# Kernel optimization log

Measured on AMD Instinct MI355X. Metric: run time of the kernel, lower is better.

Reference implementation:

```python
import jax, jax.numpy as jnp
import numpy as np

B=4; L=1024; NF=64; DM=256; DS=16; SCS=8; NL=4; DI=512; DTR=16; DC=4; NFM=6; NH=4; SCALES=(5,20,50)

def _ln(x,g,b):
    m=x.mean(-1,keepdims=True); v=((x-m)**2).mean(-1,keepdims=True)
    return (x-m)*jax.lax.rsqrt(v+1e-5)*g+b

def _scan(dA,dBu,C):
    # sequential selective scan: h_t = dA_t*h + dBu_t ; y_t = sum_n h_t * C_t
    def step(h,inp):
        a,bu,c=inp
        h=a*h+bu
        return h, jnp.einsum('bdn,bn->bd',h,c)
    h0=jnp.zeros(dA.shape[:1]+dA.shape[2:],dA.dtype)
    _,ys=jax.lax.scan(step,h0,(dA.swapaxes(0,1),dBu.swapaxes(0,1),C.swapaxes(0,1)))
    return ys.swapaxes(0,1)  # [B,L,DI]

def _mamba(x,g,b,inw,cw,cb,xpw,dtw,dtb,Alog,Dp,outw,ds):
    # MambaBlock: LN -> SelectiveSSM -> residual (dropout=identity in eval)
    xn=_ln(x,g,b)
    u,z=jnp.split(xn@inw.T,2,-1)
    k=cw.T[:,None,:]  # torch depthwise Conv1d weight [DI,1,DC] -> WIO [DC,1,DI]
    u=jax.lax.conv_general_dilated(u,k,(1,),[(cw.shape[1]-1,0)],dimension_numbers=('NWC','WIO','NWC'),feature_group_count=u.shape[-1])+cb
    u=jax.nn.silu(u)
    A=-jnp.exp(Alog)                     # [DI,ds]
    xd=u@xpw.T                           # [B,L,DTR+2*ds]
    dt=jax.nn.softplus(xd[...,:DTR]@dtw.T+dtb)   # [B,L,DI]
    Bm=xd[...,DTR:DTR+ds]; Cm=xd[...,DTR+ds:]
    dA=jnp.exp(dt[...,None]*A)                   # [B,L,DI,ds]
    dBu=dt[...,None]*Bm[:,:,None,:]*u[...,None]  # [B,L,DI,ds]
    y=_scan(dA,dBu,Cm)+u*Dp
    return x+(y*jax.nn.silu(z))@outw.T

def _mha(x,wqkv,bqkv,wout,bout):
    Bq,S,E=x.shape; hd=E//NH
    q,k,v=jnp.split(x@wqkv.T+bqkv,3,-1)
    sp=lambda t: t.reshape(Bq,S,NH,hd).transpose(0,2,1,3)
    att=jax.nn.softmax(jnp.einsum('bhqd,bhkd->bhqk',sp(q),sp(k))*(1.0/np.sqrt(hd)),-1)
    o=jnp.einsum('bhqk,bhkd->bhqd',att,sp(v)).transpose(0,2,1,3).reshape(Bq,S,E)
    return o@wout.T+bout

def _forward(x,in_w,in_b,in_ln_g,in_ln_b,mb_ln_g,mb_ln_b,mb_in_w,mb_conv_w,mb_conv_b,mb_xp_w,mb_dt_w,mb_dt_b,mb_Alog,mb_D,mb_out_w,sc_ln_g,sc_ln_b,sc_in_w,sc_conv_w,sc_conv_b,sc_xp_w,sc_dt_w,sc_dt_b,sc_Alog,sc_D,sc_out_w,fus_qkv_w,fus_qkv_b,fus_out_w,fus_out_b,ms_out_w,ms_out_b,sa_ln1_g,sa_ln1_b,sa_ln2_g,sa_ln2_b,sa_qkv_w,sa_qkv_b,sa_out_w,sa_out_b,sa_ff1_w,sa_ff1_b,sa_ff2_w,sa_ff2_b,ev1_w,ev1_b,ev2_w,ev2_b,ttf1_w,ttf1_b,ttf2_w,ttf2_b,emb_w,emb_b):
    gelu=lambda t: jax.nn.gelu(t,approximate=False)
    h=gelu(_ln(x@in_w.T+in_b,in_ln_g,in_ln_b))
    for i in range(NL):
        h=_mamba(h,mb_ln_g[i],mb_ln_b[i],mb_in_w[i],mb_conv_w[i],mb_conv_b[i],mb_xp_w[i],mb_dt_w[i],mb_dt_b[i],mb_Alog[i],mb_D[i],mb_out_w[i],DS)
    pooled=[]
    for i,s in enumerate(SCALES):
        p=_mamba(h[:,-s:,:],sc_ln_g[i],sc_ln_b[i],sc_in_w[i],sc_conv_w[i],sc_conv_b[i],sc_xp_w[i],sc_dt_w[i],sc_dt_b[i],sc_Alog[i],sc_D[i],sc_out_w[i],SCS)
        pooled.append(p.mean(1))  # AdaptiveAvgPool1d(1)
    stack=jnp.stack(pooled,1)  # [B,3,DM]
    fused=_mha(stack,fus_qkv_w,fus_qkv_b,fus_out_w,fus_out_b).reshape(x.shape[0],-1)@ms_out_w.T+ms_out_b
    s2=stack+_mha(_ln(stack,sa_ln1_g,sa_ln1_b),sa_qkv_w,sa_qkv_b,sa_out_w,sa_out_b)
    att=s2+(gelu(_ln(s2,sa_ln2_g,sa_ln2_b)@sa_ff1_w.T+sa_ff1_b)@sa_ff2_w.T+sa_ff2_b)
    final=fused+att.mean(1)
    ev=jax.nn.softplus(gelu(final@ev1_w.T+ev1_b)@ev2_w.T+ev2_b)
    alpha=ev+1.0
    Ssum=alpha.sum(-1,keepdims=True)
    probs=alpha/Ssum; unc=(NFM+1)/Ssum
    ttf=gelu(final@ttf1_w.T+ttf1_b)@ttf2_w.T+ttf2_b
    tm=jax.nn.softplus(ttf[:,:NFM]); ts=jnp.exp(0.5*ttf[:,NFM:])
    emb=final@emb_w.T+emb_b
    # concat of (probs, evidence, alpha, uncertainty, ttf_mean, ttf_std, embedding) -> [B,162]
    return jnp.concatenate([probs,ev,alpha,unc,tm,ts,emb],-1)

def setup_inputs():
    ks=iter(jax.random.split(jax.random.key(0),64))
    nk=lambda: next(ks)
    w=lambda *s: jax.random.normal(nk(),s,jnp.float32)*0.02
    z=lambda *s: jnp.zeros(s,jnp.float32)
    o=lambda *s: jnp.ones(s,jnp.float32)
    Al=lambda n,ds: jnp.broadcast_to(jnp.log(jnp.arange(1,ds+1,dtype=jnp.float32)),(n,DI,ds))
    return dict(x=jax.random.normal(nk(),(B,L,NF),jnp.float32),
        in_w=w(DM,NF), in_b=z(DM), in_ln_g=o(DM), in_ln_b=z(DM),
        mb_ln_g=o(NL,DM), mb_ln_b=z(NL,DM), mb_in_w=w(NL,2*DI,DM), mb_conv_w=w(NL,DI,DC), mb_conv_b=z(NL,DI),
        mb_xp_w=w(NL,DTR+2*DS,DI), mb_dt_w=w(NL,DI,DTR), mb_dt_b=z(NL,DI), mb_Alog=Al(NL,DS), mb_D=o(NL,DI), mb_out_w=w(NL,DM,DI),
        sc_ln_g=o(3,DM), sc_ln_b=z(3,DM), sc_in_w=w(3,2*DI,DM), sc_conv_w=w(3,DI,DC), sc_conv_b=z(3,DI),
        sc_xp_w=w(3,DTR+2*SCS,DI), sc_dt_w=w(3,DI,DTR), sc_dt_b=z(3,DI), sc_Alog=Al(3,SCS), sc_D=o(3,DI), sc_out_w=w(3,DM,DI),
        fus_qkv_w=w(3*DM,DM), fus_qkv_b=z(3*DM), fus_out_w=w(DM,DM), fus_out_b=z(DM), ms_out_w=w(DM,3*DM), ms_out_b=z(DM),
        sa_ln1_g=o(DM), sa_ln1_b=z(DM), sa_ln2_g=o(DM), sa_ln2_b=z(DM),
        sa_qkv_w=w(3*DM,DM), sa_qkv_b=z(3*DM), sa_out_w=w(DM,DM), sa_out_b=z(DM),
        sa_ff1_w=w(4*DM,DM), sa_ff1_b=z(4*DM), sa_ff2_w=w(DM,4*DM), sa_ff2_b=z(DM),
        ev1_w=w(DM,DM), ev1_b=z(DM), ev2_w=w(NFM+1,DM), ev2_b=z(NFM+1),
        ttf1_w=w(DM//2,DM), ttf1_b=z(DM//2), ttf2_w=w(2*NFM,DM//2), ttf2_b=z(2*NFM),
        emb_w=w(DM//2,DM), emb_b=z(DM//2))

def reference(x,in_w,in_b,in_ln_g,in_ln_b,mb_ln_g,mb_ln_b,mb_in_w,mb_conv_w,mb_conv_b,mb_xp_w,mb_dt_w,mb_dt_b,mb_Alog,mb_D,mb_out_w,sc_ln_g,sc_ln_b,sc_in_w,sc_conv_w,sc_conv_b,sc_xp_w,sc_dt_w,sc_dt_b,sc_Alog,sc_D,sc_out_w,fus_qkv_w,fus_qkv_b,fus_out_w,fus_out_b,ms_out_w,ms_out_b,sa_ln1_g,sa_ln1_b,sa_ln2_g,sa_ln2_b,sa_qkv_w,sa_qkv_b,sa_out_w,sa_out_b,sa_ff1_w,sa_ff1_b,sa_ff2_w,sa_ff2_b,ev1_w,ev1_b,ev2_w,ev2_b,ttf1_w,ttf1_b,ttf2_w,ttf2_b,emb_w,emb_b):
    return _forward(x,in_w,in_b,in_ln_g,in_ln_b,mb_ln_g,mb_ln_b,mb_in_w,mb_conv_w,mb_conv_b,mb_xp_w,mb_dt_w,mb_dt_b,mb_Alog,mb_D,mb_out_w,sc_ln_g,sc_ln_b,sc_in_w,sc_conv_w,sc_conv_b,sc_xp_w,sc_dt_w,sc_dt_b,sc_Alog,sc_D,sc_out_w,fus_qkv_w,fus_qkv_b,fus_out_w,fus_out_b,ms_out_w,ms_out_b,sa_ln1_g,sa_ln1_b,sa_ln2_g,sa_ln2_b,sa_qkv_w,sa_qkv_b,sa_out_w,sa_out_b,sa_ff1_w,sa_ff1_b,sa_ff2_w,sa_ff2_b,ev1_w,ev1_b,ev2_w,ev2_b,ttf1_w,ttf1_b,ttf2_w,ttf2_b,emb_w,emb_b)
```

## Files before the change

kernel.cpp:

```cpp
#include <hip/hip_runtime.h>
#include <math.h>


typedef short short8v __attribute__((ext_vector_type(8)));
typedef float f32x4   __attribute__((ext_vector_type(4)));

__device__ __forceinline__ float geluf(float x){ return 0.5f*x*(1.0f + erff(x*0.70710678118654752f)); }
__device__ __forceinline__ float softplusf_(float x){ return (x > 20.f) ? x : log1pf(expf(x)); }
__device__ __forceinline__ unsigned short f2bf(float f){
  unsigned int u = __float_as_uint(f);
  unsigned int r = (u + 0x7FFFu + ((u >> 16) & 1u)) >> 16;
  return (unsigned short)r;
}

__global__ __launch_bounds__(256) void k_f2b_all(
    const float* s0, unsigned short* d0,
    const float* s1, unsigned short* d1,
    const float* s2, unsigned short* d2,
    const float* s3, unsigned short* d3,
    const float* s4, unsigned short* d4,
    const float* s5, unsigned short* d5)
{
  int blk = blockIdx.x;
  const float* s; unsigned short* d; int base;
  if      (blk < 1024){ s=s0; d=d0; base=0; }
  else if (blk < 1536){ s=s1; d=d1; base=1024; }
  else if (blk < 1632){ s=s2; d=d2; base=1536; }
  else if (blk < 2400){ s=s3; d=d3; base=1632; }
  else if (blk < 2784){ s=s4; d=d4; base=2400; }
  else                { s=s5; d=d5; base=2784; }
  int i = ((blk - base)*256 + threadIdx.x)*4;
  float4 v = *(const float4*)(s + i);
  *(ushort4*)(d + i) = make_ushort4(f2bf(v.x), f2bf(v.y), f2bf(v.z), f2bf(v.w));
}

__global__ __launch_bounds__(256) void k_inproj(
    const float* __restrict__ x, const float* __restrict__ w,
    const float* __restrict__ b, const float* __restrict__ g,
    const float* __restrict__ beta, float* __restrict__ h)
{
  __shared__ float xr[64];
  __shared__ float r1[4], r2[4];
  int row = blockIdx.x;
  int tid = threadIdx.x;
  if (tid < 64) xr[tid] = x[row*64 + tid];
  __syncthreads();
  float acc = b[tid];
  const float* wr = w + tid*64;
  #pragma unroll
  for (int k = 0; k < 64; k++) acc += xr[k]*wr[k];
  float s1 = acc, s2 = acc*acc;
  #pragma unroll
  for (int o = 32; o > 0; o >>= 1){ s1 += __shfl_down(s1,o,64); s2 += __shfl_down(s2,o,64); }
  if ((tid & 63) == 0){ r1[tid>>6] = s1; r2[tid>>6] = s2; }
  __syncthreads();
  float S1 = r1[0]+r1[1]+r1[2]+r1[3];
  float S2 = r2[0]+r2[1]+r2[2]+r2[3];
  float m = S1*(1.f/256.f);
  float var = S2*(1.f/256.f) - m*m;
  float xn = (acc - m)*rsqrtf(var + 1e-5f)*g[tid] + beta[tid];
  h[row*256 + tid] = geluf(xn);
}

__global__ __launch_bounds__(256) void k_ln(
    const float* __restrict__ src, const float* __restrict__ g, const float* __restrict__ beta,
    unsigned short* __restrict__ dst)
{
  __shared__ float r1[4], r2[4];
  int r = blockIdx.x, tid = threadIdx.x;
  float v = src[r*256 + tid];
  float s1 = v, s2 = v*v;
  #pragma unroll
  for (int o = 32; o > 0; o >>= 1){ s1 += __shfl_down(s1,o,64); s2 += __shfl_down(s2,o,64); }
  if ((tid & 63) == 0){ r1[tid>>6] = s1; r2[tid>>6] = s2; }
  __syncthreads();
  float S1 = r1[0]+r1[1]+r1[2]+r1[3];
  float S2 = r2[0]+r2[1]+r2[2]+r2[3];
  float m = S1*(1.f/256.f);
  float var = S2*(1.f/256.f) - m*m;
  dst[r*256 + tid] = f2bf((v - m)*rsqrtf(var + 1e-5f)*g[tid] + beta[tid]);
}

__device__ __forceinline__ void sc_region(int r, int& z, int& roff, int& s){
  if (r < 64){ z=0; roff=0; s=5; }
  else if (r < 192){ z=1; roff=64; s=20; }
  else { z=2; roff=192; s=50; }
}

__global__ __launch_bounds__(256) void k_ln_sc(
    const float* __restrict__ h, const float* __restrict__ gb, const float* __restrict__ bb,
    unsigned short* __restrict__ dst)
{
  __shared__ float r1[4], r2[4];
  int r = blockIdx.x, tid = threadIdx.x;
  int z, roff, s; sc_region(r, z, roff, s);
  int local = r - roff;
  if (local >= 4*s) return;
  int b = local / s, t = local % s;
  float v = h[(b*1024 + (1024 - s) + t)*256 + tid];
  const float* g = gb + z*256; const float* be = bb + z*256;
  float s1 = v, s2 = v*v;
  #pragma unroll
  for (int o = 32; o > 0; o >>= 1){ s1 += __shfl_down(s1,o,64); s2 += __shfl_down(s2,o,64); }
  if ((tid & 63) == 0){ r1[tid>>6] = s1; r2[tid>>6] = s2; }
  __syncthreads();
  float S1 = r1[0]+r1[1]+r1[2]+r1[3];
  float S2 = r2[0]+r2[1]+r2[2]+r2[3];
  float m = S1*(1.f/256.f);
  float var = S2*(1.f/256.f) - m*m;
  dst[r*256 + tid] = f2bf((v - m)*rsqrtf(var + 1e-5f)*g[tid] + be[tid]);
}

template<int MODE, int SCB>
__global__ __launch_bounds__(256) void k_mm64(
    const unsigned short* __restrict__ A, const unsigned short* __restrict__ Wb,
    float* __restrict__ C,
    const float* __restrict__ resid,
    float* __restrict__ pool_out,
    int M, int N, int K, int wstr)
{
  int tid = threadIdx.x;
  int wave = tid >> 6, lane = tid & 63;
  int mh = wave & 1, nh = wave >> 1;
  int m0 = blockIdx.y*64 + mh*32;
  int n0 = blockIdx.x*64 + nh*32;
  int z = 0, roff = 0, sc = 0;
  const unsigned short* W = Wb;
  if (SCB){ sc_region(blockIdx.y*64, z, roff, sc); W += z*wstr; }
  int lrow = lane & 15, kc = lane >> 4;
  f32x4 acc[2][2] = {{{0.f,0.f,0.f,0.f},{0.f,0.f,0.f,0.f}},{{0.f,0.f,0.f,0.f},{0.f,0.f,0.f,0.f}}};
  for (int k0 = 0; k0 < K; k0 += 32){
    short8v a[2], b[2];
    #pragma unroll
    for (int mi = 0; mi < 2; mi++){
      int r = m0 + mi*16 + lrow; r = min(r, M-1);
      a[mi] = *(const short8v*)(A + r*K + k0 + kc*8);
    }
    #pragma unroll
    for (int ni = 0; ni < 2; ni++){
      int c = n0 + ni*16 + lrow;
      b[ni] = *(const short8v*)(W + c*K + k0 + kc*8);
    }
    #pragma unroll
    for (int mi = 0; mi < 2; mi++)
      #pragma unroll
      for (int ni = 0; ni < 2; ni++)
        acc[mi][ni] = __builtin_amdgcn_mfma_f32_16x16x32_bf16(a[mi], b[ni], acc[mi][ni], 0, 0, 0);
  }
  int rb = kc*4;
  #pragma unroll
  for (int mi = 0; mi < 2; mi++){
    #pragma unroll
    for (int rr = 0; rr < 4; rr++){
      int grow = m0 + mi*16 + rb + rr;
      if (grow >= M) continue;
      #pragma unroll
      for (int ni = 0; ni < 2; ni++){
        int gcol = n0 + ni*16 + lrow;
        float v = acc[mi][ni][rr];
        if (MODE == 0){
          C[grow*N + gcol] = v;
        } else if (MODE == 1){
          C[grow*N + gcol] = resid[grow*256 + gcol] + v;
        } else {
          int local = grow - roff;
          if (local < 4*sc){
            int bb2 = local / sc, t = local % sc;
            float rv = resid[(bb2*1024 + (1024 - sc) + t)*256 + gcol] + v;
            atomicAdd(&pool_out[bb2*768 + z*256 + gcol], rv*(1.f/(float)sc));
          }
        }
      }
    }
  }
}

template<int NT, int SCB>
__global__ __launch_bounds__(256) void k_xpdt(
    const unsigned short* __restrict__ A, const unsigned short* __restrict__ Wb,
    float* __restrict__ xdout,
    const float* __restrict__ dtwb, const float* __restrict__ dtbb,
    float* __restrict__ dtout, int M)
{
  const int K = 512;
  const int NC = NT*16;
  __shared__ float pacc[4][16][NC];
  __shared__ float sxd[16][16];
  int tid = threadIdx.x;
  int wave = tid >> 6, lane = tid & 63;
  int bm0 = blockIdx.x*16;
  const unsigned short* W = Wb;
  const float* dtw = dtwb;
  const float* dtb = dtbb;
  if (SCB){
    int z, roff, s; sc_region(bm0, z, roff, s);
    W += z*(NC*K); dtw += z*8192; dtb += z*512;
  }
  int lrow = lane & 15, kc = lane >> 4;
  int kbase = wave*128;
  f32x4 acc[NT];
  #pragma unroll
  for (int ni = 0; ni < NT; ni++) acc[ni] = (f32x4){0.f,0.f,0.f,0.f};
  #pragma unroll
  for (int k0 = 0; k0 < 128; k0 += 32){
    short8v a = *(const short8v*)(A + (bm0 + lrow)*K + kbase + k0 + kc*8);
    #pragma unroll
    for (int ni = 0; ni < NT; ni++){
      short8v b = *(const short8v*)(W + (ni*16 + lrow)*K + kbase + k0 + kc*8);
      acc[ni] = __builtin_amdgcn_mfma_f32_16x16x32_bf16(a, b, acc[ni], 0, 0, 0);
    }
  }
  int rb = kc*4;
  #pragma unroll
  for (int rr = 0; rr < 4; rr++)
    #pragma unroll
    for (int ni = 0; ni < NT; ni++)
      pacc[wave][rb + rr][ni*16 + lrow] = acc[ni][rr];
  __syncthreads();
  for (int e = tid; e < 16*NC; e += 256){
    int r = e / NC, c = e % NC;
    float v = pacc[0][r][c] + pacc[1][r][c] + pacc[2][r][c] + pacc[3][r][c];
    xdout[(bm0 + r)*NC + c] = v;
    if (c < 16) sxd[r][c] = v;
  }
  __syncthreads();
  int d0 = tid, d1 = tid + 256;
  float w0[16], w1[16];
  #pragma unroll
  for (int j = 0; j < 16; j++){ w0[j] = dtw[d0*16 + j]; w1[j] = dtw[d1*16 + j]; }
  float b0 = dtb[d0], b1 = dtb[d1];
  #pragma unroll
  for (int r = 0; r < 16; r++){
    float a0 = b0, a1 = b1;
    #pragma unroll
    for (int j = 0; j < 16; j++){
      float xv = sxd[r][j];
      a0 = fmaf(xv, w0[j], a0);
      a1 = fmaf(xv, w1[j], a1);
    }
    dtout[(bm0 + r)*512 + d0] = softplusf_(a0);
    dtout[(bm0 + r)*512 + d1] = softplusf_(a1);
  }
}

__global__ __launch_bounds__(256) void k_conv(
    const float* __restrict__ uz, const float* __restrict__ cw, const float* __restrict__ cb,
    float* __restrict__ uc, unsigned short* __restrict__ ucb)
{
  int row = blockIdx.x;
  int t = row & 1023;
  int tid = threadIdx.x;
  for (int d = tid; d < 512; d += 256){
    float acc = cb[d];
    const float* w = cw + d*4;
    #pragma unroll
    for (int k = 0; k < 4; k++){
      int ts = t - 3 + k;
      if (ts >= 0) acc += uz[(row - (3-k))*1024 + d]*w[k];
    }
    float s = acc/(1.f + expf(-acc));
    uc[row*512 + d] = s;
    ucb[row*512 + d] = f2bf(s);
  }
}

__global__ __launch_bounds__(256) void k_conv_sc(
    const float* __restrict__ uz, const float* __restrict__ cwb, const float* __restrict__ cbb,
    float* __restrict__ uc, unsigned short* __restrict__ ucb)
{
  int row = blockIdx.x;
  int z, roff, s; sc_region(row, z, roff, s);
  int local = row - roff;
  if (local >= 4*s) return;
  int t = local % s;
  const float* cw = cwb + z*2048;
  const float* cb = cbb + z*512;
  int tid = threadIdx.x;
  for (int d = tid; d < 512; d += 256){
    float acc = cb[d];
    const float* w = cw + d*4;
    #pragma unroll
    for (int k = 0; k < 4; k++){
      int ts = t - 3 + k;
      if (ts >= 0) acc += uz[(row - (3-k))*1024 + d]*w[k];
    }
    float sv = acc/(1.f + expf(-acc));
    uc[row*512 + d] = sv;
    ucb[row*512 + d] = f2bf(sv);
  }
}

__global__ __launch_bounds__(64) void k_scan_p1y(
    const float* __restrict__ dt, const float* __restrict__ uc,
    const float* __restrict__ xd, const float* __restrict__ Alog,
    float* __restrict__ hend, float* __restrict__ sdtb,
    float* __restrict__ yloc, float* __restrict__ Scum)
{
  const int CL = 64, NCH = 16;
  __shared__ float sdt[64][64], suc[64][64];
  __shared__ float sBC[64][32];
  int tid = threadIdx.x;
  int dblk = blockIdx.x;
  int d = dblk*64 + tid;
  int b = blockIdx.y, ch = blockIdx.z;
  int t0 = ch*CL;
  float A[16];
  #pragma unroll
  for (int n = 0; n < 16; n++) A[n] = -__expf(Alog[d*16 + n]);
  for (int e = tid; e < CL*16; e += 64){
    int t = e >> 4, q = (e & 15)*4;
    long off = (long)(b*1024 + t0 + t)*512 + dblk*64 + q;
    *(float4*)&sdt[t][q] = *(const float4*)(dt + off);
    *(float4*)&suc[t][q] = *(const float4*)(uc + off);
  }
  for (int e = tid; e < CL*8; e += 64){
    int t = e >> 3, q = (e & 7)*4;
    *(float4*)&sBC[t][q] = *(const float4*)(xd + (long)(b*1024 + t0 + t)*48 + 16 + q);
  }
  __syncthreads();
  float h[16];
  #pragma unroll
  for (int n = 0; n < 16; n++) h[n] = 0.f;
  float Ss = 0.f;
  #pragma unroll 2
  for (int t = 0; t < CL; t++){
    float dtv = sdt[t][tid];
    float uv  = suc[t][tid];
    Ss += dtv;
    float du = dtv*uv;
    float y = 0.f;
    #pragma unroll
    for (int n = 0; n < 16; n++){
      h[n] = fmaf(__expf(dtv*A[n]), h[n], du*sBC[t][n]);
      y = fmaf(h[n], sBC[t][16+n], y);
    }
    long row = (long)(b*1024 + t0 + t);
    yloc[row*512 + d] = y;
    Scum[row*512 + d] = Ss;
  }
  int base = ((b*NCH + ch)*512 + d)*16;
  #pragma unroll
  for (int q = 0; q < 4; q++)
    *(float4*)(hend + base + q*4) = make_float4(h[q*4], h[q*4+1], h[q*4+2], h[q*4+3]);
  sdtb[(b*NCH + ch)*512 + d] = Ss;
}

__global__ __launch_bounds__(256) void k_scomb(
    const float* __restrict__ hend, const float* __restrict__ sdtb,
    const float* __restrict__ Alog, float* __restrict__ hstart,
    float* __restrict__ Aneg)
{
  const int NCH = 16;
  int idx = blockIdx.x*256 + threadIdx.x;
  int low = idx & 8191;
  int d = (idx >> 4) & 511, b = idx >> 13;
  float A = -__expf(Alog[low]);
  if (b == 0) Aneg[low] = A;
  float hs = 0.f;
  hstart[(b*NCH)*8192 + low] = 0.f;
  for (int c = 0; c < NCH-1; c++){
    float S  = sdtb[(b*NCH + c)*512 + d];
    float he = hend[(b*NCH + c)*8192 + low];
    hs = fmaf(__expf(A*S), hs, he);
    hstart[(b*NCH + c + 1)*8192 + low] = hs;
  }
}

__global__ __launch_bounds__(256) void k_corr(
    const float* __restrict__ yloc, const float* __restrict__ Scum,
    const float* __restrict__ hstart, const float* __restrict__ Aneg,
    const float* __restrict__ xd, const float* __restrict__ uc,
    const float* __restrict__ uz, const float* __restrict__ Dp,
    unsigned short* __restrict__ yg)
{
  __shared__ float sC[16];
  int row = blockIdx.x, tid = threadIdx.x;
  int b = row >> 10, t = row & 1023, ch = t >> 6;
  if (tid < 16) sC[tid] = xd[row*48 + 32 + tid];
  __syncthreads();
  #pragma unroll
  for (int rep = 0; rep < 2; rep++){
    int d = tid + rep*256;
    float Ss = Scum[row*512 + d];
    float y  = yloc[row*512 + d];
    const float* hs = hstart + ((b*16 + ch)*512 + d)*16;
    const float* An = Aneg + d*16;
    #pragma unroll
    for (int n = 0; n < 16; n++)
      y = fmaf(__expf(An[n]*Ss)*hs[n], sC[n], y);
    float uv = uc[row*512 + d];
    y = fmaf(uv, Dp[d], y);
    float zv = uz[row*1024 + 512 + d];
    yg[row*512 + d] = f2bf(y*(zv/(1.f + __expf(-zv))));
  }
}

__global__ __launch_bounds__(64) void k_scan_sc(
    const float* __restrict__ dt, const float* __restrict__ uc,
    const float* __restrict__ uz, const float* __restrict__ xd,
    const float* __restrict__ Alogb, const float* __restrict__ Dpb,
    unsigned short* __restrict__ yg)
{
  __shared__ float sdt[52][64], suc[52][64], sz[52][64];
  __shared__ float sBC[52][16];
  int tid = threadIdx.x;
  int dblk = blockIdx.x;
  int d = dblk*64 + tid;
  int b = blockIdx.y, z = blockIdx.z;
  int s = (z==0) ? 5 : (z==1) ? 20 : 50;
  int roff = (z==0) ? 0 : (z==1) ? 64 : 192;
  const float* Alog = Alogb + z*4096;
  const float* Dp   = Dpb + z*512;
  float A[8];
  #pragma unroll
  for (int n = 0; n < 8; n++) A[n] = -__expf(Alog[d*8 + n]);
  float Dv = Dp[d];
  for (int e = tid; e < s*16; e += 64){
    int t = e >> 4, q = (e & 15)*4;
    long row = (long)(roff + b*s + t);
    *(float4*)&sdt[t][q] = *(const float4*)(dt + row*512 + dblk*64 + q);
    *(float4*)&suc[t][q] = *(const float4*)(uc + row*512 + dblk*64 + q);
    *(float4*)&sz[t][q]  = *(const float4*)(uz + row*1024 + 512 + dblk*64 + q);
  }
  for (int e = tid; e < s*4; e += 64){
    int t = e >> 2, q = (e & 3)*4;
    long row = (long)(roff + b*s + t);
    *(float4*)&sBC[t][q] = *(const float4*)(xd + row*32 + 16 + q);
  }
  __syncthreads();
  float h[8];
  #pragma unroll
  for (int n = 0; n < 8; n++) h[n] = 0.f;
  for (int t = 0; t < s; t++){
    float dtv = sdt[t][tid];
    float uv  = suc[t][tid];
    float zv  = sz[t][tid];
    float du = dtv*uv;
    float y = 0.f;
    #pragma unroll
    for (int n = 0; n < 8; n++){
      h[n] = fmaf(__expf(dtv*A[n]), h[n], du*sBC[t][n]);
      y = fmaf(h[n], sBC[t][8+n], y);
    }
    y = fmaf(uv, Dv, y);
    float gate = zv/(1.f + __expf(-zv));
    yg[(long)(roff + b*s + t)*512 + d] = f2bf(y*gate);
  }
}

__global__ void k_zero(float* p, int n){
  int i = blockIdx.x*256 + threadIdx.x;
  if (i < n) p[i] = 0.f;
}

template<int M, int ACT, int RES>
__global__ __launch_bounds__(256) void k_tw(
    const float* __restrict__ A, const float* __restrict__ W,
    const float* __restrict__ bias, float* __restrict__ out,
    const float* __restrict__ resid, int N, int K, int ostride, int ocoff)
{
  extern __shared__ float sx[];
  int tid = threadIdx.x;
  for (int e = tid*4; e < M*K; e += 1024)
    *(float4*)&sx[e] = *(const float4*)(A + e);
  __syncthreads();
  int wave = tid >> 6, lane = tid & 63;
  int c = blockIdx.x*4 + wave;
  if (c >= N) return;
  float acc[M];
  #pragma unroll
  for (int r = 0; r < M; r++) acc[r] = 0.f;
  for (int k = lane*4; k < K; k += 256){
    float4 w4 = *(const float4*)(W + c*K + k);
    #pragma unroll
    for (int r = 0; r < M; r++){
      float4 x4 = *(float4*)&sx[r*K + k];
      acc[r] = fmaf(x4.x,w4.x,fmaf(x4.y,w4.y,fmaf(x4.z,w4.z,fmaf(x4.w,w4.w,acc[r]))));
    }
  }
  #pragma unroll
  for (int r = 0; r < M; r++){
    #pragma unroll
    for (int o = 32; o > 0; o >>= 1) acc[r] += __shfl_down(acc[r], o, 64);
  }
  if (lane == 0){
    float bv = bias[c];
    #pragma unroll
    for (int r = 0; r < M; r++){
      float v = acc[r] + bv;
      if (ACT == 1) v = geluf(v);
      if (RES == 1) v += resid[r*256 + c];
      out[r*ostride + ocoff + c] = v;
    }
  }
}

__global__ __launch_bounds__(256) void k_t_ln(
    const float* __restrict__ src, const float* __restrict__ g, const float* __restrict__ b,
    float* __restrict__ dst)
{
  __shared__ float r1[4], r2[4];
  int r = blockIdx.x, tid = threadIdx.x;
  float v = src[r*256 + tid];
  float s1 = v, s2 = v*v;
  #pragma unroll
  for (int o = 32; o > 0; o >>= 1){ s1 += __shfl_down(s1,o,64); s2 += __shfl_down(s2,o,64); }
  if ((tid & 63) == 0){ r1[tid>>6] = s1; r2[tid>>6] = s2; }
  __syncthreads();
  float S1 = r1[0]+r1[1]+r1[2]+r1[3];
  float S2 = r2[0]+r2[1]+r2[2]+r2[3];
  float m = S1*(1.f/256.f);
  float var = S2*(1.f/256.f) - m*m;
  dst[r*256 + tid] = (v - m)*rsqrtf(var + 1e-5f)*g[tid] + b[tid];
}

__global__ __launch_bounds__(256) void k_t_att(
    const float* __restrict__ qkv, float* __restrict__ ov)
{
  __shared__ float att[36];
  int b = blockIdx.x, tid = threadIdx.x;
  if (tid < 36){
    int hh = tid/9, r = (tid%9)/3, c = tid%3;
    float s = 0.f;
    const float* qp = qkv + (b*3 + r)*768 + hh*64;
    const float* kp = qkv + (b*3 + c)*768 + 256 + hh*64;
    for (int k = 0; k < 64; k++) s += qp[k]*kp[k];
    att[hh*9 + r*3 + c] = s*0.125f;
  }
  __syncthreads();
  if (tid < 12){
    int hh = tid/3, r = tid%3;
    float a0 = att[hh*9+r*3+0], a1 = att[hh*9+r*3+1], a2 = att[hh*9+r*3+2];
    float m = fmaxf(a0, fmaxf(a1, a2));
    float e0 = expf(a0-m), e1 = expf(a1-m), e2 = expf(a2-m);
    float s = e0+e1+e2;
    att[hh*9+r*3+0] = e0/s; att[hh*9+r*3+1] = e1/s; att[hh*9+r*3+2] = e2/s;
  }
  __syncthreads();
  for (int e = tid; e < 768; e += 256){
    int p = e >> 8, i = e & 255, hh = i >> 6;
    ov[(b*3 + p)*256 + i] = att[hh*9+p*3+0]*qkv[(b*3+0)*768+512+i]
                          + att[hh*9+p*3+1]*qkv[(b*3+1)*768+512+i]
                          + att[hh*9+p*3+2]*qkv[(b*3+2)*768+512+i];
  }
}

__global__ __launch_bounds__(256) void k_t_final(
    const float* __restrict__ fusedv, const float* __restrict__ s2f, float* __restrict__ finalv)
{
  int b = blockIdx.x, c = threadIdx.x;
  finalv[b*256 + c] = fusedv[b*256 + c] +
    (s2f[(b*3+0)*256 + c] + s2f[(b*3+1)*256 + c] + s2f[(b*3+2)*256 + c])*(1.f/3.f);
}

__global__ __launch_bounds__(64) void k_t_fin(
    const float* __restrict__ evraw, const float* __restrict__ ttraw, float* __restrict__ out)
{
  __shared__ float ev[7];
  __shared__ float S;
  int b = blockIdx.x, tid = threadIdx.x;
  if (tid < 7) ev[tid] = softplusf_(evraw[b*7 + tid]);
  __syncthreads();
  if (tid == 0){
    float s = 0.f;
    for (int j = 0; j < 7; j++) s += ev[j] + 1.f;
    S = s;
  }
  __syncthreads();
  float* ob = out + b*162;
  if (tid < 7){
    float al = ev[tid] + 1.f;
    ob[tid] = al / S;
    ob[7 + tid] = ev[tid];
    ob[14 + tid] = al;
  }
  if (tid == 0) ob[21] = 7.f / S;
  if (tid < 6){
    ob[22 + tid] = softplusf_(ttraw[b*12 + tid]);
    ob[28 + tid] = expf(0.5f*ttraw[b*12 + 6 + tid]);
  }
}

extern "C" void kernel_launch(void* const* d_in, const int* in_sizes, int n_in,
                              void* d_out, int out_size, void* d_ws, size_t ws_size,
                              hipStream_t stream)
{
  const float* x         = (const float*)d_in[0];
  const float* in_w      = (const float*)d_in[1];
  const float* in_b      = (const float*)d_in[2];
  const float* in_ln_g   = (const float*)d_in[3];
  const float* in_ln_b   = (const float*)d_in[4];
  const float* mb_ln_g   = (const float*)d_in[5];
  const float* mb_ln_b   = (const float*)d_in[6];
  const float* mb_in_w   = (const float*)d_in[7];
  const float* mb_conv_w = (const float*)d_in[8];
  const float* mb_conv_b = (const float*)d_in[9];
  const float* mb_xp_w   = (const float*)d_in[10];
  const float* mb_dt_w   = (const float*)d_in[11];
  const float* mb_dt_b   = (const float*)d_in[12];
  const float* mb_Alog   = (const float*)d_in[13];
  const float* mb_D      = (const float*)d_in[14];
  const float* mb_out_w  = (const float*)d_in[15];
  const float* sc_ln_g   = (const float*)d_in[16];
  const float* sc_ln_b   = (const float*)d_in[17];
  const float* sc_in_w   = (const float*)d_in[18];
  const float* sc_conv_w = (const float*)d_in[19];
  const float* sc_conv_b = (const float*)d_in[20];
  const float* sc_xp_w   = (const float*)d_in[21];
  const float* sc_dt_w   = (const float*)d_in[22];
  const float* sc_dt_b   = (const float*)d_in[23];
  const float* sc_Alog   = (const float*)d_in[24];
  const float* sc_D      = (const float*)d_in[25];
  const float* sc_out_w  = (const float*)d_in[26];
  const float* fus_qkv_w = (const float*)d_in[27];
  const float* fus_qkv_b = (const float*)d_in[28];
  const float* fus_out_w = (const float*)d_in[29];
  const float* fus_out_b = (const float*)d_in[30];
  const float* ms_out_w  = (const float*)d_in[31];
  const float* ms_out_b  = (const float*)d_in[32];
  const float* sa_ln1_g  = (const float*)d_in[33];
  const float* sa_ln1_b  = (const float*)d_in[34];
  const float* sa_ln2_g  = (const float*)d_in[35];
  const float* sa_ln2_b  = (const float*)d_in[36];
  const float* sa_qkv_w  = (const float*)d_in[37];
  const float* sa_qkv_b  = (const float*)d_in[38];
  const float* sa_out_w  = (const float*)d_in[39];
  const float* sa_out_b  = (const float*)d_in[40];
  const float* sa_ff1_w  = (const float*)d_in[41];
  const float* sa_ff1_b  = (const float*)d_in[42];
  const float* sa_ff2_w  = (const float*)d_in[43];
  const float* sa_ff2_b  = (const float*)d_in[44];
  const float* ev1_w     = (const float*)d_in[45];
  const float* ev1_b     = (const float*)d_in[46];
  const float* ev2_w     = (const float*)d_in[47];
  const float* ev2_b     = (const float*)d_in[48];
  const float* ttf1_w    = (const float*)d_in[49];
  const float* ttf1_b    = (const float*)d_in[50];
  const float* ttf2_w    = (const float*)d_in[51];
  const float* ttf2_b    = (const float*)d_in[52];
  const float* emb_w     = (const float*)d_in[53];
  const float* emb_b     = (const float*)d_in[54];

  float* ws = (float*)d_ws;
  float* h     = ws;
  float* uz    = h    + 1048576;
  float* uc    = uz   + 4194304;
  float* dtb_  = uc   + 2097152;
  float* xd    = dtb_ + 2097152;
  float* stack = xd   + 196608;
  float* hend   = stack + 4096;
  float* hstart = hend + 524288;
  float* sdtb   = hstart + 524288;
  float* yloc   = sdtb + 32768;
  float* Scum   = yloc + 2097152;
  float* Aneg   = Scum + 2097152;
  float* qkvF   = Aneg + 8192;
  float* ovF    = qkvF + 9216;
  float* moF    = ovF  + 3072;
  float* fusedv = moF  + 3072;
  float* lnbuf  = fusedv + 1024;
  float* qkvS   = lnbuf + 3072;
  float* ovS    = qkvS + 9216;
  float* s2     = ovS  + 3072;
  float* ln2r   = s2   + 3072;
  float* hid    = ln2r + 3072;
  float* s2f    = hid  + 12288;
  float* finalv = s2f  + 3072;
  float* evh    = finalv + 1024;
  float* tth    = evh  + 1024;
  float* evraw  = tth  + 512;
  float* ttraw  = evraw + 32;
  float* fp32_end = ttraw + 64;
  unsigned short* bfb = (unsigned short*)fp32_end;
  unsigned short* xnb    = bfb;
  unsigned short* ucb    = xnb + 1048576;
  unsigned short* ygb    = ucb + 2097152;
  unsigned short* wmbin  = ygb + 2097152;
  unsigned short* wmbout = wmbin + 1048576;
  unsigned short* wmbxp  = wmbout + 524288;
  unsigned short* wscin  = wmbxp + 98304;
  unsigned short* wscout = wscin + 786432;
  unsigned short* wscxp  = wscout + 393216;

  k_f2b_all<<<2832, 256, 0, stream>>>(mb_in_w, wmbin, mb_out_w, wmbout, mb_xp_w, wmbxp,
                                      sc_in_w, wscin, sc_out_w, wscout, sc_xp_w, wscxp);

  k_inproj<<<4096, 256, 0, stream>>>(x, in_w, in_b, in_ln_g, in_ln_b, h);

  for (int l = 0; l < 4; l++){
    const float* Al = mb_Alog + l*8192;
    k_ln<<<4096, 256, 0, stream>>>(h, mb_ln_g + l*256, mb_ln_b + l*256, xnb);
    {
      dim3 g(16, 64);
      k_mm64<0,0><<<g, 256, 0, stream>>>(xnb, wmbin + l*262144, uz,
                                         nullptr, nullptr, 4096, 1024, 256, 0);
    }
    k_conv<<<4096, 256, 0, stream>>>(uz, mb_conv_w + l*2048, mb_conv_b + l*512, uc, ucb);
    k_xpdt<3,0><<<256, 256, 0, stream>>>(ucb, wmbxp + l*24576, xd,
                                         mb_dt_w + l*8192, mb_dt_b + l*512, dtb_, 4096);
    {
      dim3 g(8, 4, 16);
      k_scan_p1y<<<g, 64, 0, stream>>>(dtb_, uc, xd, Al, hend, sdtb, yloc, Scum);
      k_scomb<<<128, 256, 0, stream>>>(hend, sdtb, Al, hstart, Aneg);
      k_corr<<<4096, 256, 0, stream>>>(yloc, Scum, hstart, Aneg, xd, uc, uz,
                                       mb_D + l*512, ygb);
    }
    {
      dim3 g(4, 64);
      k_mm64<1,0><<<g, 256, 0, stream>>>(ygb, wmbout + l*131072, h,
                                         h, nullptr, 4096, 256, 512, 0);
    }
  }

  k_zero<<<12, 256, 0, stream>>>(stack, 3072);
  k_ln_sc<<<448, 256, 0, stream>>>(h, sc_ln_g, sc_ln_b, xnb);
  {
    dim3 g(16, 7);
    k_mm64<0,1><<<g, 256, 0, stream>>>(xnb, wscin, uz, nullptr, nullptr,
                                       448, 1024, 256, 262144);
  }
  k_conv_sc<<<448, 256, 0, stream>>>(uz, sc_conv_w, sc_conv_b, uc, ucb);
  k_xpdt<2,1><<<28, 256, 0, stream>>>(ucb, wscxp, xd, sc_dt_w, sc_dt_b, dtb_, 448);
  {
    dim3 g(8, 4, 3);
    k_scan_sc<<<g, 64, 0, stream>>>(dtb_, uc, uz, xd, sc_Alog, sc_D, ygb);
  }
  {
    dim3 g(4, 7);
    k_mm64<2,1><<<g, 256, 0, stream>>>(ygb, wscout, nullptr, h, stack,
                                       448, 256, 512, 131072);
  }

  float* dout = (float*)d_out;
  k_tw<12,0,0><<<192, 256, 12*256*4, stream>>>(stack, fus_qkv_w, fus_qkv_b, qkvF, nullptr, 768, 256, 768, 0);
  k_t_att<<<4, 256, 0, stream>>>(qkvF, ovF);
  k_tw<12,0,0><<<64, 256, 12*256*4, stream>>>(ovF, fus_out_w, fus_out_b, moF, nullptr, 256, 256, 256, 0);
  k_tw<4,0,0><<<64, 256, 4*768*4, stream>>>(moF, ms_out_w, ms_out_b, fusedv, nullptr, 256, 768, 256, 0);
  k_t_ln<<<12, 256, 0, stream>>>(stack, sa_ln1_g, sa_ln1_b, lnbuf);
  k_tw<12,0,0><<<192, 256, 12*256*4, stream>>>(lnbuf, sa_qkv_w, sa_qkv_b, qkvS, nullptr, 768, 256, 768, 0);
  k_t_att<<<4, 256, 0, stream>>>(qkvS, ovS);
  k_tw<12,0,1><<<64, 256, 12*256*4, stream>>>(ovS, sa_out_w, sa_out_b, s2, stack, 256, 256, 256, 0);
  k_t_ln<<<12, 256, 0, stream>>>(s2, sa_ln2_g, sa_ln2_b, ln2r);
  k_tw<12,1,0><<<256, 256, 12*256*4, stream>>>(ln2r, sa_ff1_w, sa_ff1_b, hid, nullptr, 1024, 256, 1024, 0);
  k_tw<12,0,1><<<64, 256, 12*1024*4, stream>>>(hid, sa_ff2_w, sa_ff2_b, s2f, s2, 256, 1024, 256, 0);
  k_t_final<<<4, 256, 0, stream>>>(fusedv, s2f, finalv);
  k_tw<4,1,0><<<64, 256, 4*256*4, stream>>>(finalv, ev1_w, ev1_b, evh, nullptr, 256, 256, 256, 0);
  k_tw<4,0,0><<<2, 256, 4*256*4, stream>>>(evh, ev2_w, ev2_b, evraw, nullptr, 7, 256, 7, 0);
  k_tw<4,1,0><<<32, 256, 4*256*4, stream>>>(finalv, ttf1_w, ttf1_b, tth, nullptr, 128, 256, 128, 0);
  k_tw<4,0,0><<<3, 256, 4*128*4, stream>>>(tth, ttf2_w, ttf2_b, ttraw, nullptr, 12, 128, 12, 0);
  k_tw<4,0,0><<<32, 256, 4*256*4, stream>>>(finalv, emb_w, emb_b, dout, nullptr, 128, 256, 162, 34);
  k_t_fin<<<4, 64, 0, stream>>>(evraw, ttraw, dout);
}
```

Measured before the change: 735.7 us.

## Fuse depthwise conv+SiLU into x-proj/dt kernel and fold stack zeroing into LN

The causal depthwise conv and SiLU are now computed inside the x-projection/dt kernel, with the bf16 activations staged in shared memory instead of written to and reread from a global bf16 buffer. This removes one launch per layer and a global round trip. The separate zeroing kernel is folded into extra blocks of the scale LN kernel. The scan phase-1 kernel now uses 256 threads for the cooperative shared-memory loads, but only 64 threads run the recurrence, so three waves sit idle during the scan. The fused kernel has only 256 blocks doing the conv work that the standalone conv kernel spread over 4096 blocks, which may reduce parallelism.

```diff
diff --git a/kernel.cpp b/kernel.cpp
--- a/kernel.cpp
+++ b/kernel.cpp
@@ -11,6 +11,12 @@
   unsigned int u = __float_as_uint(f);
   unsigned int r = (u + 0x7FFFu + ((u >> 16) & 1u)) >> 16;
   return (unsigned short)r;
+}
+
+__device__ __forceinline__ void sc_region(int r, int& z, int& roff, int& s){
+  if (r < 64){ z=0; roff=0; s=5; }
+  else if (r < 192){ z=1; roff=64; s=20; }
+  else { z=2; roff=192; s=50; }
 }
 
 __global__ __launch_bounds__(256) void k_f2b_all(
@@ -81,18 +87,17 @@
   dst[r*256 + tid] = f2bf((v - m)*rsqrtf(var + 1e-5f)*g[tid] + beta[tid]);
 }
 
-__device__ __forceinline__ void sc_region(int r, int& z, int& roff, int& s){
-  if (r < 64){ z=0; roff=0; s=5; }
-  else if (r < 192){ z=1; roff=64; s=20; }
-  else { z=2; roff=192; s=50; }
-}
-
 __global__ __launch_bounds__(256) void k_ln_sc(
     const float* __restrict__ h, const float* __restrict__ gb, const float* __restrict__ bb,
-    unsigned short* __restrict__ dst)
+    unsigned short* __restrict__ dst, float* __restrict__ stack)
 {
   __shared__ float r1[4], r2[4];
   int r = blockIdx.x, tid = threadIdx.x;
+  if (r >= 448){
+    int idx = (r - 448)*256 + tid;
+    if (idx < 3072) stack[idx] = 0.f;
+    return;
+  }
   int z, roff, s; sc_region(r, z, roff, s);
   int local = r - roff;
   if (local >= 4*s) return;
@@ -176,14 +181,17 @@
 }
 
 template<int NT, int SCB>
-__global__ __launch_bounds__(256) void k_xpdt(
-    const unsigned short* __restrict__ A, const unsigned short* __restrict__ Wb,
-    float* __restrict__ xdout,
+__global__ __launch_bounds__(256) void k_cxpdt(
+    const float* __restrict__ uz,
+    const float* __restrict__ cwb, const float* __restrict__ cbb,
+    float* __restrict__ uc,
+    const unsigned short* __restrict__ Wb, float* __restrict__ xdout,
     const float* __restrict__ dtwb, const float* __restrict__ dtbb,
-    float* __restrict__ dtout, int M)
+    float* __restrict__ dtout)
 {
   const int K = 512;
   const int NC = NT*16;
+  __shared__ unsigned short sucb[16][520];
   __shared__ float pacc[4][16][NC];
   __shared__ float sxd[16][16];
   int tid = threadIdx.x;
@@ -192,10 +200,40 @@
   const unsigned short* W = Wb;
   const float* dtw = dtwb;
   const float* dtb = dtbb;
+  const float* cw0 = cwb;
+  const float* cb0 = cbb;
   if (SCB){
     int z, roff, s; sc_region(bm0, z, roff, s);
     W += z*(NC*K); dtw += z*8192; dtb += z*512;
-  }
+    cw0 = cwb + z*2048; cb0 = cbb + z*512;
+  }
+  for (int e = tid; e < 16*512; e += 256){
+    int r = e >> 9, d = e & 511;
+    int row = bm0 + r;
+    int t; bool valid = true;
+    if (SCB){
+      int z, roff, s; sc_region(row, z, roff, s);
+      int local = row - roff;
+      valid = local < 4*s;
+      t = valid ? (local % s) : 0;
+    } else {
+      t = row & 1023;
+    }
+    float sv = 0.f;
+    if (valid){
+      float acc = cb0[d];
+      const float* w = cw0 + d*4;
+      #pragma unroll
+      for (int k = 0; k < 4; k++){
+        int ts = t - 3 + k;
+        if (ts >= 0) acc += uz[(long)(row - (3-k))*1024 + d]*w[k];
+      }
+      sv = acc/(1.f + expf(-acc));
+    }
+    uc[(long)row*512 + d] = sv;
+    sucb[r][d] = f2bf(sv);
+  }
+  __syncthreads();
   int lrow = lane & 15, kc = lane >> 4;
   int kbase = wave*128;
   f32x4 acc[NT];
@@ -203,7 +241,7 @@
   for (int ni = 0; ni < NT; ni++) acc[ni] = (f32x4){0.f,0.f,0.f,0.f};
   #pragma unroll
   for (int k0 = 0; k0 < 128; k0 += 32){
-    short8v a = *(const short8v*)(A + (bm0 + lrow)*K + kbase + k0 + kc*8);
+    short8v a = *(const short8v*)&sucb[lrow][kbase + k0 + kc*8];
     #pragma unroll
     for (int ni = 0; ni < NT; ni++){
       short8v b = *(const short8v*)(W + (ni*16 + lrow)*K + kbase + k0 + kc*8);
@@ -243,54 +281,7 @@
   }
 }
 
-__global__ __launch_bounds__(256) void k_conv(
-    const float* __restrict__ uz, const float* __restrict__ cw, const float* __restrict__ cb,
-    float* __restrict__ uc, unsigned short* __restrict__ ucb)
-{
-  int row = blockIdx.x;
-  int t = row & 1023;
-  int tid = threadIdx.x;
-  for (int d = tid; d < 512; d += 256){
-    float acc = cb[d];
-    const float* w = cw + d*4;
-    #pragma unroll
-    for (int k = 0; k < 4; k++){
-      int ts = t - 3 + k;
-      if (ts >= 0) acc += uz[(row - (3-k))*1024 + d]*w[k];
-    }
-    float s = acc/(1.f + expf(-acc));
-    uc[row*512 + d] = s;
-    ucb[row*512 + d] = f2bf(s);
-  }
-}
-
-__global__ __launch_bounds__(256) void k_conv_sc(
-    const float* __restrict__ uz, const float* __restrict__ cwb, const float* __restrict__ cbb,
-    float* __restrict__ uc, unsigned short* __restrict__ ucb)
-{
-  int row = blockIdx.x;
-  int z, roff, s; sc_region(row, z, roff, s);
-  int local = row - roff;
-  if (local >= 4*s) return;
-  int t = local % s;
-  const float* cw = cwb + z*2048;
-  const float* cb = cbb + z*512;
-  int tid = threadIdx.x;
-  for (int d = tid; d < 512; d += 256){
-    float acc = cb[d];
-    const float* w = cw + d*4;
-    #pragma unroll
-    for (int k = 0; k < 4; k++){
-      int ts = t - 3 + k;
-      if (ts >= 0) acc += uz[(row - (3-k))*1024 + d]*w[k];
-    }
-    float sv = acc/(1.f + expf(-acc));
-    uc[row*512 + d] = sv;
-    ucb[row*512 + d] = f2bf(sv);
-  }
-}
-
-__global__ __launch_bounds__(64) void k_scan_p1y(
+__global__ __launch_bounds__(256) void k_scan_p1y(
     const float* __restrict__ dt, const float* __restrict__ uc,
     const float* __restrict__ xd, const float* __restrict__ Alog,
     float* __restrict__ hend, float* __restrict__ sdtb,
@@ -301,48 +292,50 @@
   __shared__ float sBC[64][32];
   int tid = threadIdx.x;
   int dblk = blockIdx.x;
-  int d = dblk*64 + tid;
   int b = blockIdx.y, ch = blockIdx.z;
   int t0 = ch*CL;
-  float A[16];
-  #pragma unroll
-  for (int n = 0; n < 16; n++) A[n] = -__expf(Alog[d*16 + n]);
-  for (int e = tid; e < CL*16; e += 64){
+  for (int e = tid; e < CL*16; e += 256){
     int t = e >> 4, q = (e & 15)*4;
     long off = (long)(b*1024 + t0 + t)*512 + dblk*64 + q;
     *(float4*)&sdt[t][q] = *(const float4*)(dt + off);
     *(float4*)&suc[t][q] = *(const float4*)(uc + off);
   }
-  for (int e = tid; e < CL*8; e += 64){
+  for (int e = tid; e < CL*8; e += 256){
     int t = e >> 3, q = (e & 7)*4;
     *(float4*)&sBC[t][q] = *(const float4*)(xd + (long)(b*1024 + t0 + t)*48 + 16 + q);
   }
   __syncthreads();
-  float h[16];
-  #pragma unroll
-  for (int n = 0; n < 16; n++) h[n] = 0.f;
-  float Ss = 0.f;
-  #pragma unroll 2
-  for (int t = 0; t < CL; t++){
-    float dtv = sdt[t][tid];
-    float uv  = suc[t][tid];
-    Ss += dtv;
-    float du = dtv*uv;
-    float y = 0.f;
-    #pragma unroll
-    for (int n = 0; n < 16; n++){
-      h[n] = fmaf(__expf(dtv*A[n]), h[n], du*sBC[t][n]);
-      y = fmaf(h[n], sBC[t][16+n], y);
-    }
-    long row = (long)(b*1024 + t0 + t);
-    yloc[row*512 + d] = y;
-    Scum[row*512 + d] = Ss;
-  }
-  int base = ((b*NCH + ch)*512 + d)*16;
-  #pragma unroll
-  for (int q = 0; q < 4; q++)
-    *(float4*)(hend + base + q*4) = make_float4(h[q*4], h[q*4+1], h[q*4+2], h[q*4+3]);
-  sdtb[(b*NCH + ch)*512 + d] = Ss;
+  if (tid < 64){
+    int d = dblk*64 + tid;
+    float A[16];
+    #pragma unroll
+    for (int n = 0; n < 16; n++) A[n] = -__expf(Alog[d*16 + n]);
+    float h[16];
+    #pragma unroll
+    for (int n = 0; n < 16; n++) h[n] = 0.f;
+    float Ss = 0.f;
+    #pragma unroll 2
+    for (int t = 0; t < CL; t++){
+      float dtv = sdt[t][tid];
+      float uv  = suc[t][tid];
+      Ss += dtv;
+      float du = dtv*uv;
+      float y = 0.f;
+      #pragma unroll
+      for (int n = 0; n < 16; n++){
+        h[n] = fmaf(__expf(dtv*A[n]), h[n], du*sBC[t][n]);
+        y = fmaf(h[n], sBC[t][16+n], y);
+      }
+      long row = (long)(b*1024 + t0 + t);
+      yloc[row*512 + d] = y;
+      Scum[row*512 + d] = Ss;
+    }
+    int base = ((b*NCH + ch)*512 + d)*16;
+    #pragma unroll
+    for (int q = 0; q < 4; q++)
+      *(float4*)(hend + base + q*4) = make_float4(h[q*4], h[q*4+1], h[q*4+2], h[q*4+3]);
+    sdtb[(b*NCH + ch)*512 + d] = Ss;
+  }
 }
 
 __global__ __launch_bounds__(256) void k_scomb(
@@ -390,7 +383,7 @@
       y = fmaf(__expf(An[n]*Ss)*hs[n], sC[n], y);
     float uv = uc[row*512 + d];
     y = fmaf(uv, Dp[d], y);
-    float zv = uz[row*1024 + 512 + d];
+    float zv = uz[(long)row*1024 + 512 + d];
     yg[row*512 + d] = f2bf(y*(zv/(1.f + __expf(-zv))));
   }
 }
@@ -446,11 +439,6 @@
     float gate = zv/(1.f + __expf(-zv));
     yg[(long)(roff + b*s + t)*512 + d] = f2bf(y*gate);
   }
-}
-
-__global__ void k_zero(float* p, int n){
-  int i = blockIdx.x*256 + threadIdx.x;
-  if (i < n) p[i] = 0.f;
 }
 
 template<int M, int ACT, int RES>
@@ -673,8 +661,7 @@
   float* fp32_end = ttraw + 64;
   unsigned short* bfb = (unsigned short*)fp32_end;
   unsigned short* xnb    = bfb;
-  unsigned short* ucb    = xnb + 1048576;
-  unsigned short* ygb    = ucb + 2097152;
+  unsigned short* ygb    = xnb + 1048576;
   unsigned short* wmbin  = ygb + 2097152;
   unsigned short* wmbout = wmbin + 1048576;
   unsigned short* wmbxp  = wmbout + 524288;
@@ -695,12 +682,12 @@
       k_mm64<0,0><<<g, 256, 0, stream>>>(xnb, wmbin + l*262144, uz,
                                          nullptr, nullptr, 4096, 1024, 256, 0);
     }
-    k_conv<<<4096, 256, 0, stream>>>(uz, mb_conv_w + l*2048, mb_conv_b + l*512, uc, ucb);
-    k_xpdt<3,0><<<256, 256, 0, stream>>>(ucb, wmbxp + l*24576, xd,
-                                         mb_dt_w + l*8192, mb_dt_b + l*512, dtb_, 4096);
+    k_cxpdt<3,0><<<256, 256, 0, stream>>>(uz, mb_conv_w + l*2048, mb_conv_b + l*512, uc,
+                                          wmbxp + l*24576, xd,
+                                          mb_dt_w + l*8192, mb_dt_b + l*512, dtb_);
     {
       dim3 g(8, 4, 16);
-      k_scan_p1y<<<g, 64, 0, stream>>>(dtb_, uc, xd, Al, hend, sdtb, yloc, Scum);
+      k_scan_p1y<<<g, 256, 0, stream>>>(dtb_, uc, xd, Al, hend, sdtb, yloc, Scum);
       k_scomb<<<128, 256, 0, stream>>>(hend, sdtb, Al, hstart, Aneg);
       k_corr<<<4096, 256, 0, stream>>>(yloc, Scum, hstart, Aneg, xd, uc, uz,
                                        mb_D + l*512, ygb);
@@ -712,15 +699,14 @@
     }
   }
 
-  k_zero<<<12, 256, 0, stream>>>(stack, 3072);
-  k_ln_sc<<<448, 256, 0, stream>>>(h, sc_ln_g, sc_ln_b, xnb);
+  k_ln_sc<<<460, 256, 0, stream>>>(h, sc_ln_g, sc_ln_b, xnb, stack);
   {
     dim3 g(16, 7);
     k_mm64<0,1><<<g, 256, 0, stream>>>(xnb, wscin, uz, nullptr, nullptr,
                                        448, 1024, 256, 262144);
   }
-  k_conv_sc<<<448, 256, 0, stream>>>(uz, sc_conv_w, sc_conv_b, uc, ucb);
-  k_xpdt<2,1><<<28, 256, 0, stream>>>(ucb, wscxp, xd, sc_dt_w, sc_dt_b, dtb_, 448);
+  k_cxpdt<2,1><<<28, 256, 0, stream>>>(uz, sc_conv_w, sc_conv_b, uc,
+                                       wscxp, xd, sc_dt_w, sc_dt_b, dtb_);
   {
     dim3 g(8, 4, 3);
     k_scan_sc<<<g, 64, 0, stream>>>(dtb_, uc, uz, xd, sc_Alog, sc_D, ygb);
```

Result: slower. 799.4 us (+8.7%).
